# Performance work log

Hardware: AMD Instinct MI355X
Metric: run time of the kernel (lower is better)

The kernel has to match this reference:

```python
import jax, jax.numpy as jnp
import numpy as np

WS = 7        # kernel_size
DIL = 1       # dilation
HEADS = 8


def _reflect(idx, L):
    # stnls-style reflect bounds (no edge duplication): -1 -> 1, L -> L-2
    period = 2 * (L - 1)
    m = jnp.mod(idx, period)
    return jnp.where(m > L - 1, period - m, m)


def setup_inputs() -> dict:
    key = jax.random.key(0)
    k1, k2, k3 = jax.random.split(key, 3)
    T, H, W, C = 8, 64, 64, 256
    x = jax.random.normal(k1, (T, H, W, C), jnp.float32)
    # flows: (1, T, 2*wt, 2, H, W) with wt=1; channel 0 = di (rows), 1 = dj (cols)
    flows = jax.random.normal(k2, (1, T, 2, 2, H, W), jnp.float32) * 2.0
    W_qk = jax.random.normal(k3, (2 * C, C), jnp.float32) * 0.02
    return {"x": x, "flows": flows, "W_qk": W_qk}


def _slot(q, k, tp, fli, flj):
    # q,k: (HD,T,H,W,hd); tp: (T,) frame index per query frame; fli,flj: (T,H,W) flow
    HD, T, H, W, hd = q.shape
    di = jnp.round(fli).astype(jnp.int32)   # itype='int': integer flow offsets
    dj = jnp.round(flj).astype(jnp.int32)
    ci = jnp.arange(H, dtype=jnp.int32)[None, :, None] + di   # (T,H,W) window centers
    cj = jnp.arange(W, dtype=jnp.int32)[None, None, :] + dj
    kg = k[:, tp]                                             # (HD,T,H,W,hd) keys of searched frame
    off = DIL * (jnp.arange(WS, dtype=jnp.int32) - WS // 2)
    t_idx = jnp.arange(T)[:, None, None, None]
    ii = jnp.arange(H, dtype=jnp.int32)[None, :, None]
    jj = jnp.arange(W, dtype=jnp.int32)[None, None, :, None]
    dt = (tp - jnp.arange(T)).astype(jnp.int32)               # (T,)
    scores, offs = [], []
    for a in range(WS):  # structural loop over window rows to bound intermediates
        li = _reflect(ci + off[a], H)                                    # (T,H,W)
        lj = _reflect(cj[..., None] + off[None, None, None, :], W)       # (T,H,W,WS)
        kn = kg[:, t_idx, li[..., None], lj, :]                          # (HD,T,H,W,WS,hd)
        scores.append(jnp.einsum('dthwf,dthwbf->dthwb', q, kn))         # (HD,T,H,W,WS)
        o = jnp.stack([
            jnp.broadcast_to(dt[:, None, None, None], (T, H, W, WS)),
            jnp.broadcast_to((li - ii[:, :, :]) [..., None], (T, H, W, WS)),
            lj - jj], axis=-1)                                           # (T,H,W,WS,3)
        offs.append(o)
    s = jnp.stack(scores, axis=4).reshape(HD, T, H, W, WS * WS)
    o = jnp.stack(offs, axis=3).reshape(T, H, W, WS * WS, 3)
    return s, o


def reference(x, flows, W_qk):
    T, H, W, C = x.shape
    hd = C // HEADS
    scale = hd ** (-0.5)
    qk = (x @ W_qk.T).reshape(T, H, W, 2, HEADS, hd)
    q = jnp.transpose(qk[:, :, :, 0], (3, 0, 1, 2, 4))  # (HD,T,H,W,hd)
    k = jnp.transpose(qk[:, :, :, 1], (3, 0, 1, 2, 4))
    t = jnp.arange(T)
    tp1 = jnp.where(t + 1 < T, t + 1, t - 2)   # forward frame, window shifted at boundary
    tp2 = jnp.where(t - 1 >= 0, t - 1, t + 2)  # backward frame
    z = jnp.zeros((T, H, W), x.dtype)
    s0, o0 = _slot(q, k, t, z, z)
    s1, o1 = _slot(q, k, tp1, flows[0, :, 0, 0], flows[0, :, 0, 1])
    s2, o2 = _slot(q, k, tp2, flows[0, :, 1, 0], flows[0, :, 1, 1])
    attn = scale * jnp.concatenate([s0, s1, s2], axis=-1)[None]   # (1,HD,T,H,W,K)
    fk = jnp.concatenate([o0, o1, o2], axis=3)                    # (T,H,W,K,3)
    flows_k = jnp.broadcast_to(fk[None, None], (1, HEADS) + fk.shape)
    return attn, flows_k
```

## Files before the change

### kernel.cpp

```cpp
#include <hip/hip_runtime.h>
#include <hip/hip_bf16.h>

#define TT_    8
#define HEADS_ 8
#define NB_    147
#define NPIX   32768
#define NTASK  (NPIX*NB_)
#define ROWS_  (NPIX + 512)

typedef _Float16 half8 __attribute__((ext_vector_type(8)));
typedef _Float16 h2    __attribute__((ext_vector_type(2)));
typedef float    f32x4 __attribute__((ext_vector_type(4)));

__device__ __forceinline__ int reflect64(int v) {
  int m = v % 126;
  m += (m >> 31) & 126;
  return (m > 63) ? (126 - m) : m;
}

__device__ __forceinline__ float dot2f(h2 a, h2 b, float c) {
#if __has_builtin(__builtin_amdgcn_fdot2)
  return __builtin_amdgcn_fdot2(a, b, c, false);
#else
  return c + (float)a[0]*(float)b[0] + (float)a[1]*(float)b[1];
#endif
}

__device__ __forceinline__ float dpp_xor1(float x) {
  int r = __builtin_amdgcn_mov_dpp(__builtin_bit_cast(int, x), 0xB1, 0xF, 0xF, true);
  return __builtin_bit_cast(float, r);
}
__device__ __forceinline__ float dpp_xor2(float x) {
  int r = __builtin_amdgcn_mov_dpp(__builtin_bit_cast(int, x), 0x4E, 0xF, 0xF, true);
  return __builtin_bit_cast(float, r);
}

__global__ __launch_bounds__(256) void prepack(
    const float* __restrict__ x, const float* __restrict__ wqk,
    _Float16* __restrict__ outp) {
  int o  = (int)blockIdx.x * 256 + (int)threadIdx.x;
  int r  = o & 15, quad = (o >> 4) & 3, ks = (o >> 6) & 7, mt = o >> 9;
  int row = mt * 16 + r;
  const float* src = (row < NPIX) ? (x + (size_t)row * 256)
                                  : (wqk + (size_t)(row - NPIX) * 256);
  int col = (ks * 4 + quad) * 8;
  float4 a = *(const float4*)(src + col);
  float4 b = *(const float4*)(src + col + 4);
  half8 h;
  h[0]=(_Float16)a.x; h[1]=(_Float16)a.y; h[2]=(_Float16)a.z; h[3]=(_Float16)a.w;
  h[4]=(_Float16)b.x; h[5]=(_Float16)b.y; h[6]=(_Float16)b.z; h[7]=(_Float16)b.w;
  ((half8*)outp)[o] = h;
}

__global__ __launch_bounds__(256) void qk_gemm(
    const _Float16* __restrict__ Ap,
    _Float16* __restrict__ qws, _Float16* __restrict__ kws) {
  const half8* A8 = (const half8*)Ap;
  const half8* B8 = (const half8*)(Ap + (size_t)NPIX * 256);
  int bid  = (int)blockIdx.x;
  int mblk = bid >> 3, nblk = bid & 7;
  int lane = (int)threadIdx.x & 63, wv = (int)threadIdx.x >> 6;
  int wm = mblk * 64 + (wv >> 1) * 32;
  int wn = nblk * 64 + (wv & 1) * 32;
  int r = lane & 15, quad = lane >> 4;

  half8 af[2][8], bf[2][8];
#pragma unroll
  for (int im = 0; im < 2; im++) {
    int mt = (wm >> 4) + im;
#pragma unroll
    for (int ks = 0; ks < 8; ks++)
      af[im][ks] = A8[((mt * 8 + ks) * 4 + quad) * 16 + r];
  }
#pragma unroll
  for (int in = 0; in < 2; in++) {
    int nt = (wn >> 4) + in;
#pragma unroll
    for (int ks = 0; ks < 8; ks++)
      bf[in][ks] = B8[((nt * 8 + ks) * 4 + quad) * 16 + r];
  }

  f32x4 acc[2][2] = {};
#pragma unroll
  for (int ks = 0; ks < 8; ks++)
#pragma unroll
    for (int im = 0; im < 2; im++)
#pragma unroll
      for (int in = 0; in < 2; in++)
        acc[im][in] = __builtin_amdgcn_mfma_f32_16x16x32_f16(
            af[im][ks], bf[in][ks], acc[im][in], 0, 0, 0);

  _Float16* dst = (wn < 256) ? qws : kws;
  int nsub = (wn < 256) ? 0 : 256;
#pragma unroll
  for (int im = 0; im < 2; im++)
#pragma unroll
    for (int in = 0; in < 2; in++) {
      int n = wn + in * 16 + r - nsub;
#pragma unroll
      for (int reg = 0; reg < 4; reg++) {
        int m = wm + im * 16 + quad * 4 + reg;
        dst[(size_t)m * 256 + n] = (_Float16)acc[im][in][reg];
      }
    }
}

__global__ __launch_bounds__(256) void attn_kernel(
    const float* __restrict__ flows,
    const _Float16* __restrict__ qws, const _Float16* __restrict__ kws,
    float* __restrict__ out) {
  __shared__ int      s_info[256];
  __shared__ __attribute__((aligned(16))) _Float16 s_q[3 * 32 * 8];
  __shared__ __attribute__((aligned(16))) float    s_attn[8 * 260];
  __shared__ __attribute__((aligned(16))) float    s_flow[768];

  int nbq = (int)gridDim.x >> 3;
  int blk = ((int)blockIdx.x & 7) * nbq + ((int)blockIdx.x >> 3);
  int tx  = (int)threadIdx.x;
  int btid0 = blk * 256;
  int p0 = (int)((unsigned)btid0 / 147u);

  {
    int tid = btid0 + tx;
    unsigned p = (unsigned)tid / 147u;
    int nb = tid - (int)(p * 147u);
    int t = (int)(p >> 12), hw = (int)(p & 4095u);
    int h = hw >> 6, w = hw & 63;
    int slot = nb / 49;
    int rr = nb - slot * 49;
    int a = rr / 7, b = rr - a * 7;
    int tp = t, di = 0, dj = 0;
    if (slot > 0) {
      int si = slot - 1;
      di = (int)rintf(flows[(size_t)((t * 2 + si) * 2 + 0) * 4096 + hw]);
      dj = (int)rintf(flows[(size_t)((t * 2 + si) * 2 + 1) * 4096 + hw]);
      tp = (slot == 1) ? ((t + 1 < TT_) ? t + 1 : t - 2)
                       : ((t - 1 >= 0)  ? t - 1 : t + 2);
    }
    int li = reflect64(h + di + a - 3);
    int lj = reflect64(w + dj + b - 3);
    int kidx = (tp << 12) + (li << 6) + lj;
    int pixloc = (int)p - p0;
    s_info[tx] = kidx | (pixloc << 20);
    s_flow[tx * 3 + 0] = (float)(tp - t);
    s_flow[tx * 3 + 1] = (float)(li - h);
    s_flow[tx * 3 + 2] = (float)(lj - w);
  }
  if (tx < 96) {
    int pix = tx >> 5, s = tx & 31;
    int p = p0 + pix; if (p > NPIX - 1) p = NPIX - 1;
    half8 v = *(const half8*)(qws + (size_t)p * 256 + s * 8);
    ((half8*)s_q)[pix * 32 + s] = v;
  }
  __syncthreads();

  int lane = tx & 63, wv = tx >> 6;
  int j = lane & 7, g = lane >> 3;
  const float scale = 0.17677669529663687f;
#pragma unroll
  for (int it = 0; it < 8; it++) {
    int tb = wv * 64 + it * 8 + g;
    int info = s_info[tb];
    int kidx = info & 0xFFFFF;
    int pixloc = info >> 20;
    const half8* kp = (const half8*)(kws + ((size_t)kidx << 8)) + j;
    const half8* qp = ((const half8*)s_q) + pixloc * 32 + j;
    float acc[4];
#pragma unroll
    for (int c = 0; c < 4; c++) {
      half8 k8 = kp[c * 8];
      half8 q8 = qp[c * 8];
      float s = 0.f;
#pragma unroll
      for (int u = 0; u < 8; u += 2) {
        h2 ka = { k8[u], k8[u + 1] };
        h2 qa = { q8[u], q8[u + 1] };
        s = dot2f(ka, qa, s);
      }
      acc[c] = s;
    }
#pragma unroll
    for (int c = 0; c < 4; c++) {
      float t = acc[c];
      t += dpp_xor1(t);
      t += dpp_xor2(t);
      if ((lane & 3) == 0)
        s_attn[(2 * c + ((lane >> 2) & 1)) * 260 + tb] = t * scale;
    }
  }
  __syncthreads();

  const f32x4* sa4 = (const f32x4*)s_attn;
#pragma unroll
  for (int o = 0; o < 2; o++) {
    int gg = tx + o * 256;
    int hh = gg >> 6, idx = gg & 63;
    f32x4 v = sa4[hh * 65 + idx];
    __builtin_nontemporal_store(v, (f32x4*)(out + (size_t)hh * NTASK + btid0) + idx);
  }
  float* fo = out + (size_t)HEADS_ * NTASK;
  const f32x4* sf4 = (const f32x4*)s_flow;
#pragma unroll
  for (int o = 0; o < 6; o++) {
    int gg = tx + o * 256;
    int hh = gg / 192, idx = gg - hh * 192;
    f32x4 v = sf4[idx];
    __builtin_nontemporal_store(v, (f32x4*)(fo + (size_t)hh * NTASK * 3 + (size_t)btid0 * 3) + idx);
  }
}

extern "C" void kernel_launch(void* const* d_in, const int* in_sizes, int n_in,
                              void* d_out, int out_size, void* d_ws, size_t ws_size,
                              hipStream_t stream) {
  const float* x     = (const float*)d_in[0];
  const float* flows = (const float*)d_in[1];
  const float* wqk   = (const float*)d_in[2];
  float* out = (float*)d_out;

  _Float16* qws = (_Float16*)d_ws;
  _Float16* kws = qws + (size_t)NPIX * 256;
  _Float16* Ap  = kws + (size_t)NPIX * 256;

  prepack<<<dim3(ROWS_ * 32 / 256), dim3(256), 0, stream>>>(x, wqk, Ap);
  qk_gemm<<<dim3(4096), dim3(256), 0, stream>>>(Ap, qws, kws);
  attn_kernel<<<dim3(NTASK / 256), dim3(256), 0, stream>>>(flows, qws, kws, out);
}
```

Measured before the change: 680.5 us.

## Split attention heads across two block halves mapped per XCD

Launches twice as many attention blocks. Each block handles 4 of the 8 heads (one half of the channels) for its 256 tasks, and the block index is remapped so each XCD group works on a contiguous slice with a fixed head half. This is meant to shrink the K working set each XCD's L2 sees and to raise parallelism. In exchange, the index/flow setup and the flow-output writes are now done redundantly by both halves, and each block stores only half of the flow outputs.

```diff
diff --git a/kernel.cpp b/kernel.cpp
--- a/kernel.cpp
+++ b/kernel.cpp
@@ -7,6 +7,7 @@
 #define NPIX   32768
 #define NTASK  (NPIX*NB_)
 #define ROWS_  (NPIX + 512)
+#define NBLK_SLICE 2352
 
 typedef _Float16 half8 __attribute__((ext_vector_type(8)));
 typedef _Float16 h2    __attribute__((ext_vector_type(2)));
@@ -110,13 +111,19 @@
     const _Float16* __restrict__ qws, const _Float16* __restrict__ kws,
     float* __restrict__ out) {
   __shared__ int      s_info[256];
-  __shared__ __attribute__((aligned(16))) _Float16 s_q[3 * 32 * 8];
-  __shared__ __attribute__((aligned(16))) float    s_attn[8 * 260];
+  __shared__ __attribute__((aligned(16))) _Float16 s_q[3 * 16 * 8];
+  __shared__ __attribute__((aligned(16))) float    s_attn[4 * 260];
   __shared__ __attribute__((aligned(16))) float    s_flow[768];
 
-  int nbq = (int)gridDim.x >> 3;
-  int blk = ((int)blockIdx.x & 7) * nbq + ((int)blockIdx.x >> 3);
-  int tx  = (int)threadIdx.x;
+  int i    = (int)blockIdx.x;
+  int xcd  = i & 7;
+  int r_   = i >> 3;
+  int half = xcd >> 2;
+  int hi   = (r_ >= NBLK_SLICE) ? 1 : 0;
+  int slice = 2 * (xcd & 3) + hi;
+  int q_   = r_ - hi * NBLK_SLICE;
+  int blk  = slice * NBLK_SLICE + q_;
+  int tx   = (int)threadIdx.x;
   int btid0 = blk * 256;
   int p0 = (int)((unsigned)btid0 / 147u);
 
@@ -146,11 +153,11 @@
     s_flow[tx * 3 + 1] = (float)(li - h);
     s_flow[tx * 3 + 2] = (float)(lj - w);
   }
-  if (tx < 96) {
-    int pix = tx >> 5, s = tx & 31;
+  if (tx < 48) {
+    int pix = tx >> 4, s = tx & 15;
     int p = p0 + pix; if (p > NPIX - 1) p = NPIX - 1;
-    half8 v = *(const half8*)(qws + (size_t)p * 256 + s * 8);
-    ((half8*)s_q)[pix * 32 + s] = v;
+    half8 v = *(const half8*)(qws + (size_t)p * 256 + (half * 16 + s) * 8);
+    ((half8*)s_q)[pix * 16 + s] = v;
   }
   __syncthreads();
 
@@ -163,13 +170,13 @@
     int info = s_info[tb];
     int kidx = info & 0xFFFFF;
     int pixloc = info >> 20;
-    const half8* kp = (const half8*)(kws + ((size_t)kidx << 8)) + j;
-    const half8* qp = ((const half8*)s_q) + pixloc * 32 + j;
-    float acc[4];
-#pragma unroll
-    for (int c = 0; c < 4; c++) {
-      half8 k8 = kp[c * 8];
-      half8 q8 = qp[c * 8];
+    const half8* kp = (const half8*)(kws + ((size_t)kidx << 8)) + half * 16 + j;
+    const half8* qp = ((const half8*)s_q) + pixloc * 16 + j;
+    float acc[2];
+#pragma unroll
+    for (int cc = 0; cc < 2; cc++) {
+      half8 k8 = kp[cc * 8];
+      half8 q8 = qp[cc * 8];
       float s = 0.f;
 #pragma unroll
       for (int u = 0; u < 8; u += 2) {
@@ -177,35 +184,35 @@
         h2 qa = { q8[u], q8[u + 1] };
         s = dot2f(ka, qa, s);
       }
-      acc[c] = s;
-    }
-#pragma unroll
-    for (int c = 0; c < 4; c++) {
-      float t = acc[c];
+      acc[cc] = s;
+    }
+#pragma unroll
+    for (int cc = 0; cc < 2; cc++) {
+      float t = acc[cc];
       t += dpp_xor1(t);
       t += dpp_xor2(t);
       if ((lane & 3) == 0)
-        s_attn[(2 * c + ((lane >> 2) & 1)) * 260 + tb] = t * scale;
+        s_attn[(2 * cc + ((lane >> 2) & 1)) * 260 + tb] = t * scale;
     }
   }
   __syncthreads();
 
   const f32x4* sa4 = (const f32x4*)s_attn;
-#pragma unroll
-  for (int o = 0; o < 2; o++) {
-    int gg = tx + o * 256;
-    int hh = gg >> 6, idx = gg & 63;
+  {
+    int hh = tx >> 6, idx = tx & 63;
     f32x4 v = sa4[hh * 65 + idx];
-    __builtin_nontemporal_store(v, (f32x4*)(out + (size_t)hh * NTASK + btid0) + idx);
+    __builtin_nontemporal_store(v,
+        (f32x4*)(out + (size_t)(half * 4 + hh) * NTASK + btid0) + idx);
   }
   float* fo = out + (size_t)HEADS_ * NTASK;
   const f32x4* sf4 = (const f32x4*)s_flow;
 #pragma unroll
-  for (int o = 0; o < 6; o++) {
+  for (int o = 0; o < 3; o++) {
     int gg = tx + o * 256;
     int hh = gg / 192, idx = gg - hh * 192;
     f32x4 v = sf4[idx];
-    __builtin_nontemporal_store(v, (f32x4*)(fo + (size_t)hh * NTASK * 3 + (size_t)btid0 * 3) + idx);
+    __builtin_nontemporal_store(v,
+        (f32x4*)(fo + (size_t)(half * 4 + hh) * NTASK * 3 + (size_t)btid0 * 3) + idx);
   }
 }
 
@@ -223,5 +230,5 @@
 
   prepack<<<dim3(ROWS_ * 32 / 256), dim3(256), 0, stream>>>(x, wqk, Ap);
   qk_gemm<<<dim3(4096), dim3(256), 0, stream>>>(Ap, qws, kws);
-  attn_kernel<<<dim3(NTASK / 256), dim3(256), 0, stream>>>(flows, qws, kws, out);
-}
+  attn_kernel<<<dim3(2 * NTASK / 256), dim3(256), 0, stream>>>(flows, qws, kws, out);
+}
```

After: 719.7 us. +5.8%, slower.
